# Kernel tuning notes

Measured on AMD Instinct MI355X. Metric: run time of the kernel, lower is better.

Reference implementation:

```python
import jax, jax.numpy as jnp
import numpy as np
from jax import lax

B, T, D, L, H, F = 2, 128, 256, 8, 4, 2048  # batch, time, dim, max_chunk_len, nhead, dim_feedforward
THRESH = 0.5


def setup_inputs() -> dict:
    key = jax.random.key(0)
    ks = jax.random.split(key, 12)
    s = 0.02
    nrm = lambda k, sh, sc=s: jax.random.normal(k, sh, jnp.float32) * sc
    return {
        "frames": jax.random.normal(ks[0], (B, T, D), jnp.float32),
        "cls_token": jax.random.normal(ks[1], (D,), jnp.float32),
        "Wq": nrm(ks[2], (D, D)), "bq": jnp.zeros((D,), jnp.float32),
        "Wk": nrm(ks[3], (D, D)), "bk": jnp.zeros((D,), jnp.float32),
        "Wv": nrm(ks[4], (D, D)), "bv": jnp.zeros((D,), jnp.float32),
        "Wo": nrm(ks[5], (D, D)), "bo": jnp.zeros((D,), jnp.float32),
        "ln1_g": jnp.ones((D,), jnp.float32), "ln1_b": jnp.zeros((D,), jnp.float32),
        "ln2_g": jnp.ones((D,), jnp.float32), "ln2_b": jnp.zeros((D,), jnp.float32),
        "W1": nrm(ks[6], (D, F)), "b1f": jnp.zeros((F,), jnp.float32),
        "W2": nrm(ks[7], (F, D)), "b2f": jnp.zeros((D,), jnp.float32),
        "We1": nrm(ks[8], (D, D)), "be1": jnp.zeros((D,), jnp.float32),
        "We2": jax.random.normal(ks[9], (D,), jnp.float32) * 0.1,
        "be2": jnp.zeros((), jnp.float32),
    }


def reference(frames, cls_token, Wq, bq, Wk, bk, Wv, bv, Wo, bo,
              ln1_g, ln1_b, ln2_g, ln2_b, W1, b1f, W2, b2f,
              We1, be1, We2, be2):
    """Dynamic chunker: for each start index i, grow window 1..L over frames[i:],
    run a pre-norm TransformerEncoderLayer on [CLS, window], stop at first
    p_eoc > THRESH (or window cap). Emits CLS encodings per chunk.
    Returns (chunks [B,T,D] zero-padded, counts [B])."""
    Bq, Tq, Dq = frames.shape
    dh = Dq // H
    scale = 1.0 / np.sqrt(dh).astype(np.float32)

    def ln(x, g, b):
        m = jnp.mean(x, -1, keepdims=True)
        v = jnp.var(x, -1, keepdims=True)
        return (x - m) * lax.rsqrt(v + 1e-5) * g + b

    def enc_cls(seq, kp):
        # seq: (1+L, D); kp: (1+L,) True = padded key. norm_first encoder layer.
        S = seq.shape[0]
        h = ln(seq, ln1_g, ln1_b)
        q = (h @ Wq + bq).reshape(S, H, dh)
        k = (h @ Wk + bk).reshape(S, H, dh)
        v = (h @ Wv + bv).reshape(S, H, dh)
        scores = jnp.einsum('qhd,khd->hqk', q, k) * scale
        scores = jnp.where(kp[None, None, :], -1e30, scores)
        a = jax.nn.softmax(scores, axis=-1)
        o = jnp.einsum('hqk,khd->qhd', a, v).reshape(S, Dq)
        x = seq + o @ Wo + bo
        h2 = ln(x, ln2_g, ln2_b)
        x = x + jax.nn.relu(h2 @ W1 + b1f) @ W2 + b2f
        return x[0]  # CLS position

    pos = jnp.arange(L)
    ls = jnp.arange(1, L + 1)

    def run(fpad):  # fpad: (T+L, D), one sample
        def step(i, _):
            win = lax.dynamic_slice(fpad, (i, 0), (L, Dq))           # frames[i:i+L] (zero-padded past T)
            seq = jnp.concatenate([cls_token[None, :], win], 0)     # (1+L, D)
            base_pad = (i + pos) >= Tq                               # positions past end of sequence
            kp = jnp.concatenate(
                [jnp.zeros((L, 1), bool),
                 (pos[None, :] >= ls[:, None]) | base_pad[None, :]], 1)  # (L, 1+L) one mask per candidate len
            enc = jax.vmap(enc_cls, in_axes=(None, 0))(seq, kp)      # (L, D) candidate CLS encodings
            p = jax.nn.sigmoid(jax.nn.relu(enc @ We1 + be1) @ We2 + be2)  # (L,) eoc probs
            lmax = jnp.clip(Tq - i, 1, L)
            stop = (p > THRESH) & (ls <= lmax)
            lstar = jnp.where(stop.any(), jnp.argmax(stop) + 1, lmax)
            active = i < Tq
            chunk = jnp.where(active, enc[lstar - 1], jnp.zeros((Dq,), seq.dtype))
            i_new = jnp.where(active, i + lstar.astype(i.dtype), i)
            return i_new, (chunk, active)

        _, (chunks, act) = lax.scan(step, jnp.int32(0), None, length=Tq)
        return chunks, act

    fpadded = jnp.pad(frames, ((0, 0), (0, L), (0, 0)))
    chunks, act = jax.vmap(run)(fpadded)
    counts = act.sum(-1).astype(jnp.int32)
    return chunks, counts
```

## Files before the change

kernel.cpp:

```cpp
#include <hip/hip_runtime.h>

#define DEV __device__ __forceinline__

constexpr int Bc = 2, Tc = 128, Dc = 256, Lc = 8, Hc = 4, DH = 64, Fc = 2048;
constexpr float EPS = 1e-5f, SCALE = 0.125f;
constexpr int NROWS = Bc * Tc * Lc;
constexpr int SLAB = NROWS * Dc;

constexpr int OFF_K     = 0;
constexpr int OFF_VWOH  = OFF_K + Bc * Tc * Dc;
constexpr int OFF_QCLS  = OFF_VWOH + Bc * Tc * Hc * Dc;
constexpr int OFF_KCLS  = OFF_QCLS + Dc;
constexpr int OFF_VWOHC = OFF_KCLS + Dc;
constexpr int OFF_X0    = OFF_VWOHC + Hc * Dc;
constexpr int OFF_ENC   = OFF_X0;
constexpr int OFF_H2    = OFF_X0 + SLAB;
constexpr int OFF_UP    = OFF_H2 + SLAB;
constexpr int OFF_Z     = OFF_UP + 4 * SLAB;

DEV int imin(int a, int b) { return a < b ? a : b; }

DEV float blockReduceSum(float v, float* red) {
#pragma unroll
  for (int off = 32; off; off >>= 1) v += __shfl_down(v, off, 64);
  const int lane = threadIdx.x & 63;
  const int w = threadIdx.x >> 6;
  __syncthreads();
  if (lane == 0) red[w] = v;
  __syncthreads();
  return red[0] + red[1] + red[2] + red[3];
}

__global__ __launch_bounds__(256) void k_prep(
    const float* __restrict__ frames, const float* __restrict__ cls,
    const float* __restrict__ Wq, const float* __restrict__ bq,
    const float* __restrict__ Wk, const float* __restrict__ bk,
    const float* __restrict__ Wv, const float* __restrict__ bv,
    const float* __restrict__ Wo,
    const float* __restrict__ g1, const float* __restrict__ b1,
    float* __restrict__ ws) {
  __shared__ float hsm[Dc];
  __shared__ float vsm[Dc];
  __shared__ float red[4];
  const int d = threadIdx.x;
  const int r = blockIdx.x;

  const float x = (r < Bc * Tc) ? frames[r * Dc + d] : cls[d];
  const float s = blockReduceSum(x, red);
  const float m = s * (1.0f / Dc);
  const float c = x - m;
  const float var = blockReduceSum(c * c, red) * (1.0f / Dc);
  hsm[d] = c * (1.0f / sqrtf(var + EPS)) * g1[d] + b1[d];
  __syncthreads();

  float ka = bk[d], va = bv[d];
  for (int c2 = 0; c2 < Dc; ++c2) {
    const float h = hsm[c2];
    ka = fmaf(h, Wk[c2 * Dc + d], ka);
    va = fmaf(h, Wv[c2 * Dc + d], va);
  }
  if (r < Bc * Tc) ws[OFF_K + r * Dc + d] = ka;
  else             ws[OFF_KCLS + d] = ka;
  vsm[d] = va;
  __syncthreads();

#pragma unroll
  for (int hh = 0; hh < Hc; ++hh) {
    float acc = 0.f;
    for (int c2 = 0; c2 < DH; ++c2)
      acc = fmaf(vsm[hh * DH + c2], Wo[(hh * DH + c2) * Dc + d], acc);
    if (r < Bc * Tc) ws[OFF_VWOH + r * (Hc * Dc) + hh * Dc + d] = acc;
    else             ws[OFF_VWOHC + hh * Dc + d] = acc;
  }
  if (r == Bc * Tc) {
    float qa = bq[d];
    for (int c2 = 0; c2 < Dc; ++c2) qa = fmaf(hsm[c2], Wq[c2 * Dc + d], qa);
    ws[OFF_QCLS + d] = qa;
  }
}

__global__ __launch_bounds__(256) void k_attn(
    const float* __restrict__ cls, const float* __restrict__ bo,
    const float* __restrict__ g2, const float* __restrict__ b2,
    float* __restrict__ ws) {
  const int wg = blockIdx.x;
  const int i = wg & (Tc - 1);
  const int d = threadIdx.x;
  const int lmax = imin(Tc - i, Lc);
  __shared__ float sv[Hc][Lc + 1];
  __shared__ float aP[Lc][Hc][Lc + 1];
  __shared__ __align__(16) float redA[Lc][4];
  __shared__ __align__(16) float redB[Lc][4];

  const int hh = d >> 6, lane = d & 63;
  {
    const float qv = ws[OFF_QCLS + hh * DH + lane];
    for (int j = 0; j <= Lc; ++j) {
      float p = 0.f;
      if (j == 0) p = qv * ws[OFF_KCLS + hh * DH + lane];
      else if (j - 1 < lmax) p = qv * ws[OFF_K + (wg + j - 1) * Dc + hh * DH + lane];
#pragma unroll
      for (int off = 32; off; off >>= 1) p += __shfl_down(p, off, 64);
      if (lane == 0) sv[hh][j] = p * SCALE;
    }
  }
  __syncthreads();

  if (d < Lc * Hc) {
    const int l = (d >> 2) + 1, h4 = d & 3;
    if (l <= lmax) {
      float mx = -1e30f;
      for (int j = 0; j <= l; ++j) mx = fmaxf(mx, sv[h4][j]);
      float den = 0.f;
      for (int j = 0; j <= l; ++j) den += expf(sv[h4][j] - mx);
      const float inv = 1.f / den;
      for (int j = 0; j <= l; ++j) aP[l - 1][h4][j] = expf(sv[h4][j] - mx) * inv;
    }
  }
  __syncthreads();

  float x0v[Lc];
  const float base = cls[d] + bo[d];
#pragma unroll
  for (int l = 0; l < Lc; ++l) x0v[l] = base;
  for (int j = 0; j <= lmax; ++j) {
    const float* vw = (j == 0) ? (ws + OFF_VWOHC)
                               : (ws + OFF_VWOH + (wg + j - 1) * (Hc * Dc));
    for (int h4 = 0; h4 < Hc; ++h4) {
      const float w = vw[h4 * Dc + d];
      const int lstart = (j == 0) ? 1 : j;
      for (int l = lstart; l <= lmax; ++l) x0v[l - 1] = fmaf(aP[l - 1][h4][j], w, x0v[l - 1]);
    }
  }

#pragma unroll
  for (int l = 0; l < Lc; ++l) {
    float p = x0v[l];
#pragma unroll
    for (int off = 32; off; off >>= 1) p += __shfl_down(p, off, 64);
    if (lane == 0) redA[l][hh] = p;
  }
  __syncthreads();
  float mean[Lc];
#pragma unroll
  for (int l = 0; l < Lc; ++l) {
    const float4 s4 = *(const float4*)redA[l];
    mean[l] = (s4.x + s4.y + s4.z + s4.w) * (1.f / Dc);
  }
#pragma unroll
  for (int l = 0; l < Lc; ++l) {
    const float cv = x0v[l] - mean[l];
    float p = cv * cv;
#pragma unroll
    for (int off = 32; off; off >>= 1) p += __shfl_down(p, off, 64);
    if (lane == 0) redB[l][hh] = p;
  }
  __syncthreads();

  const float g2d = g2[d], b2d = b2[d];
  for (int l = 1; l <= lmax; ++l) {
    const float4 s4 = *(const float4*)redB[l - 1];
    const float var = (s4.x + s4.y + s4.z + s4.w) * (1.f / Dc);
    const float rstd = 1.f / sqrtf(var + EPS);
    const float h2 = (x0v[l - 1] - mean[l - 1]) * rstd * g2d + b2d;
    const int rowc = wg * Lc + l - 1;
    ws[OFF_X0 + rowc * Dc + d] = x0v[l - 1];
    ws[OFF_H2 + rowc * Dc + d] = h2;
  }
  for (int l = lmax + 1; l <= Lc; ++l) {
    const int rowc = wg * Lc + l - 1;
    ws[OFF_X0 + rowc * Dc + d] = 0.f;
    ws[OFF_H2 + rowc * Dc + d] = 0.f;
  }
}

__global__ __launch_bounds__(256) void k_ffn(
    const float* __restrict__ W1, const float* __restrict__ b1f,
    const float* __restrict__ W2, float* __restrict__ ws) {
  const int mtile = blockIdx.x >> 2;
  const int q = blockIdx.x & 3;
  const int r0 = mtile * 16;
  const int tid = threadIdx.x;
  __shared__ float h2s[16][Dc];
  __shared__ float ts[16][512];

  {
    const int row = tid >> 4, c0 = (tid & 15) * 16;
    const float* src = ws + OFF_H2 + (r0 + row) * Dc + c0;
#pragma unroll
    for (int j = 0; j < 4; ++j)
      *(float4*)&h2s[row][c0 + 4 * j] = *(const float4*)&src[4 * j];
  }

  const int mg = tid >> 6;
  const int lane = tid & 63;
  const int fA = q * 512 + lane * 4;
  const int fB = fA + 256;

  float t[4][8];
  {
    const float4 bA = *(const float4*)&b1f[fA];
    const float4 bB = *(const float4*)&b1f[fB];
#pragma unroll
    for (int r = 0; r < 4; ++r) {
      t[r][0] = bA.x; t[r][1] = bA.y; t[r][2] = bA.z; t[r][3] = bA.w;
      t[r][4] = bB.x; t[r][5] = bB.y; t[r][6] = bB.z; t[r][7] = bB.w;
    }
  }
  for (int c = 0; c < Dc; c += 4) {
    float4 wA[4], wB[4];
#pragma unroll
    for (int k = 0; k < 4; ++k) {
      wA[k] = *(const float4*)&W1[(c + k) * Fc + fA];
      wB[k] = *(const float4*)&W1[(c + k) * Fc + fB];
    }
#pragma unroll
    for (int r = 0; r < 4; ++r) {
      const float4 h = *(const float4*)&h2s[mg * 4 + r][c];
      const float hv[4] = {h.x, h.y, h.z, h.w};
#pragma unroll
      for (int k = 0; k < 4; ++k) {
        t[r][0] = fmaf(hv[k], wA[k].x, t[r][0]);
        t[r][1] = fmaf(hv[k], wA[k].y, t[r][1]);
        t[r][2] = fmaf(hv[k], wA[k].z, t[r][2]);
        t[r][3] = fmaf(hv[k], wA[k].w, t[r][3]);
        t[r][4] = fmaf(hv[k], wB[k].x, t[r][4]);
        t[r][5] = fmaf(hv[k], wB[k].y, t[r][5]);
        t[r][6] = fmaf(hv[k], wB[k].z, t[r][6]);
        t[r][7] = fmaf(hv[k], wB[k].w, t[r][7]);
      }
    }
  }
#pragma unroll
  for (int r = 0; r < 4; ++r) {
    float4 vA, vB;
    vA.x = fmaxf(t[r][0], 0.f); vA.y = fmaxf(t[r][1], 0.f);
    vA.z = fmaxf(t[r][2], 0.f); vA.w = fmaxf(t[r][3], 0.f);
    vB.x = fmaxf(t[r][4], 0.f); vB.y = fmaxf(t[r][5], 0.f);
    vB.z = fmaxf(t[r][6], 0.f); vB.w = fmaxf(t[r][7], 0.f);
    *(float4*)&ts[mg * 4 + r][lane * 4] = vA;
    *(float4*)&ts[mg * 4 + r][256 + lane * 4] = vB;
  }

  const int d4 = lane * 4;
  float u[4][4];
#pragma unroll
  for (int r = 0; r < 4; ++r) { u[r][0] = 0.f; u[r][1] = 0.f; u[r][2] = 0.f; u[r][3] = 0.f; }
  for (int k = 0; k < 512; k += 4) {
    float4 wv[4];
#pragma unroll
    for (int kk = 0; kk < 4; ++kk)
      wv[kk] = *(const float4*)&W2[(q * 512 + k + kk) * Dc + d4];
#pragma unroll
    for (int r = 0; r < 4; ++r) {
      const float4 h = *(const float4*)&ts[mg * 4 + r][k];
      const float hv[4] = {h.x, h.y, h.z, h.w};
#pragma unroll
      for (int kk = 0; kk < 4; ++kk) {
        u[r][0] = fmaf(hv[kk], wv[kk].x, u[r][0]);
        u[r][1] = fmaf(hv[kk], wv[kk].y, u[r][1]);
        u[r][2] = fmaf(hv[kk], wv[kk].z, u[r][2]);
        u[r][3] = fmaf(hv[kk], wv[kk].w, u[r][3]);
      }
    }
  }
  float* up = ws + OFF_UP + q * SLAB;
#pragma unroll
  for (int r = 0; r < 4; ++r) {
    float4 v; v.x = u[r][0]; v.y = u[r][1]; v.z = u[r][2]; v.w = u[r][3];
    *(float4*)&up[(r0 + mg * 4 + r) * Dc + d4] = v;
  }
}

__global__ __launch_bounds__(256) void k_encz(
    const float* __restrict__ We1, const float* __restrict__ be1,
    const float* __restrict__ We2, const float* __restrict__ be2,
    const float* __restrict__ b2f, float* __restrict__ ws) {
  const int r0 = blockIdx.x * 8;
  const int f = threadIdx.x;
  __shared__ float encs[8][Dc];
  __shared__ __align__(16) float red[8][4];
  const float bb = b2f[f];
#pragma unroll
  for (int r = 0; r < 8; ++r) {
    const int row = r0 + r;
    const float e = ws[OFF_X0 + row * Dc + f] +
                    ws[OFF_UP + 0 * SLAB + row * Dc + f] +
                    ws[OFF_UP + 1 * SLAB + row * Dc + f] +
                    ws[OFF_UP + 2 * SLAB + row * Dc + f] +
                    ws[OFF_UP + 3 * SLAB + row * Dc + f] + bb;
    ws[OFF_ENC + row * Dc + f] = e;
    encs[r][f] = e;
  }
  __syncthreads();

  float g[8];
  const float be1f = be1[f];
#pragma unroll
  for (int r = 0; r < 8; ++r) g[r] = be1f;
  for (int c = 0; c < Dc; ++c) {
    const float w = We1[c * Dc + f];
#pragma unroll
    for (int r = 0; r < 8; ++r) g[r] = fmaf(encs[r][c], w, g[r]);
  }
  const float w2 = We2[f];
  const int lane = f & 63, wv = f >> 6;
#pragma unroll
  for (int r = 0; r < 8; ++r) {
    float p = fmaxf(g[r], 0.f) * w2;
#pragma unroll
    for (int off = 32; off; off >>= 1) p += __shfl_down(p, off, 64);
    if (lane == 0) red[r][wv] = p;
  }
  __syncthreads();
  if (f < 8) {
    const float4 s4 = *(const float4*)red[f];
    ws[OFF_Z + r0 + f] = s4.x + s4.y + s4.z + s4.w + be2[0];
  }
}

__global__ __launch_bounds__(256) void k_emit(float* __restrict__ ws, float* __restrict__ out) {
  const int b = blockIdx.x;
  const int tid = threadIdx.x;
  __shared__ int lst[Tc];
  __shared__ int path[Tc];
  __shared__ int cnt_s;
  if (tid < Tc) {
    const int i = tid;
    const int lmax = imin(Tc - i, Lc);
    const float* z = ws + OFF_Z + (b * Tc + i) * Lc;
    int ls = lmax;
    for (int l = 1; l <= lmax; ++l) {
      if (z[l - 1] > 0.f) { ls = l; break; }
    }
    lst[tid] = ls;
  }
  __syncthreads();
  if (tid < 64) {
    const int a0 = lst[tid], a1 = lst[64 + tid];
    int cur = 0, s = 0;
    while (cur < Tc) {
      const int l = (cur < 64) ? __shfl(a0, cur, 64) : __shfl(a1, cur - 64, 64);
      if (tid == 0) path[s] = cur * Lc + l - 1;
      ++s;
      cur += l;
    }
    if (tid == 0) cnt_s = s;
  }
  __syncthreads();
  const int c = cnt_s;
  for (int s0 = 0; s0 < Tc; s0 += 8) {
    float v[8];
#pragma unroll
    for (int k = 0; k < 8; ++k) {
      const int s = s0 + k;
      v[k] = (s < c) ? ws[OFF_ENC + (b * Tc * Lc + path[s]) * Dc + tid] : 0.f;
    }
#pragma unroll
    for (int k = 0; k < 8; ++k) out[(b * Tc + s0 + k) * Dc + tid] = v[k];
  }
  if (tid == 0) out[Bc * Tc * Dc + b] = (float)c;
}

extern "C" void kernel_launch(void* const* d_in, const int* in_sizes, int n_in,
                              void* d_out, int out_size, void* d_ws, size_t ws_size,
                              hipStream_t stream) {
  const float* frames = (const float*)d_in[0];
  const float* cls    = (const float*)d_in[1];
  const float* Wq     = (const float*)d_in[2];
  const float* bq     = (const float*)d_in[3];
  const float* Wk     = (const float*)d_in[4];
  const float* bk     = (const float*)d_in[5];
  const float* Wv     = (const float*)d_in[6];
  const float* bv     = (const float*)d_in[7];
  const float* Wo     = (const float*)d_in[8];
  const float* bo     = (const float*)d_in[9];
  const float* g1     = (const float*)d_in[10];
  const float* b1     = (const float*)d_in[11];
  const float* g2     = (const float*)d_in[12];
  const float* b2     = (const float*)d_in[13];
  const float* W1     = (const float*)d_in[14];
  const float* b1f    = (const float*)d_in[15];
  const float* W2     = (const float*)d_in[16];
  const float* b2f    = (const float*)d_in[17];
  const float* We1    = (const float*)d_in[18];
  const float* be1    = (const float*)d_in[19];
  const float* We2    = (const float*)d_in[20];
  const float* be2    = (const float*)d_in[21];
  float* ws = (float*)d_ws;
  float* out = (float*)d_out;

  k_prep<<<Bc * Tc + 1, 256, 0, stream>>>(frames, cls, Wq, bq, Wk, bk, Wv, bv, Wo, g1, b1, ws);
  k_attn<<<Bc * Tc, 256, 0, stream>>>(cls, bo, g2, b2, ws);
  k_ffn<<<512, 256, 0, stream>>>(W1, b1f, W2, ws);
  k_encz<<<NROWS / 8, 256, 0, stream>>>(We1, be1, We2, be2, b2f, ws);
  k_emit<<<Bc, 256, 0, stream>>>(ws, out);
}
```

Measured before the change: 253.9 us.

## Fuse FFN and end-of-chunk head into one kernel with in-block reduction

Merges the FFN kernel and the encoder/EOC-score kernel into a single 512-thread kernel. Each block now handles 8 rows over the full 2048-wide hidden dimension, where before four blocks each took a 512-wide quarter of 16 rows. The partial W2 sums are reduced in shared memory, so the four 'UP' partial slabs no longer round-trip through global memory and one launch disappears. In exchange, each block streams all of W1 and W2 for only 8 rows, so weight reuse per block is halved, and per-thread register pressure goes up.

```diff
diff --git a/kernel.cpp b/kernel.cpp
--- a/kernel.cpp
+++ b/kernel.cpp
@@ -15,8 +15,7 @@
 constexpr int OFF_X0    = OFF_VWOHC + Hc * Dc;
 constexpr int OFF_ENC   = OFF_X0;
 constexpr int OFF_H2    = OFF_X0 + SLAB;
-constexpr int OFF_UP    = OFF_H2 + SLAB;
-constexpr int OFF_Z     = OFF_UP + 4 * SLAB;
+constexpr int OFF_Z     = OFF_H2 + SLAB;
 
 DEV int imin(int a, int b) { return a < b ? a : b; }
 
@@ -174,148 +173,150 @@
   }
 }
 
-__global__ __launch_bounds__(256) void k_ffn(
+__global__ __launch_bounds__(512) void k_ffn(
     const float* __restrict__ W1, const float* __restrict__ b1f,
-    const float* __restrict__ W2, float* __restrict__ ws) {
-  const int mtile = blockIdx.x >> 2;
-  const int q = blockIdx.x & 3;
-  const int r0 = mtile * 16;
-  const int tid = threadIdx.x;
-  __shared__ float h2s[16][Dc];
-  __shared__ float ts[16][512];
-
-  {
-    const int row = tid >> 4, c0 = (tid & 15) * 16;
-    const float* src = ws + OFF_H2 + (r0 + row) * Dc + c0;
-#pragma unroll
-    for (int j = 0; j < 4; ++j)
-      *(float4*)&h2s[row][c0 + 4 * j] = *(const float4*)&src[4 * j];
-  }
-
-  const int mg = tid >> 6;
-  const int lane = tid & 63;
-  const int fA = q * 512 + lane * 4;
-  const int fB = fA + 256;
-
-  float t[4][8];
-  {
-    const float4 bA = *(const float4*)&b1f[fA];
-    const float4 bB = *(const float4*)&b1f[fB];
-#pragma unroll
-    for (int r = 0; r < 4; ++r) {
-      t[r][0] = bA.x; t[r][1] = bA.y; t[r][2] = bA.z; t[r][3] = bA.w;
-      t[r][4] = bB.x; t[r][5] = bB.y; t[r][6] = bB.z; t[r][7] = bB.w;
-    }
-  }
-  for (int c = 0; c < Dc; c += 4) {
-    float4 wA[4], wB[4];
-#pragma unroll
-    for (int k = 0; k < 4; ++k) {
-      wA[k] = *(const float4*)&W1[(c + k) * Fc + fA];
-      wB[k] = *(const float4*)&W1[(c + k) * Fc + fB];
-    }
-#pragma unroll
-    for (int r = 0; r < 4; ++r) {
-      const float4 h = *(const float4*)&h2s[mg * 4 + r][c];
-      const float hv[4] = {h.x, h.y, h.z, h.w};
-#pragma unroll
-      for (int k = 0; k < 4; ++k) {
-        t[r][0] = fmaf(hv[k], wA[k].x, t[r][0]);
-        t[r][1] = fmaf(hv[k], wA[k].y, t[r][1]);
-        t[r][2] = fmaf(hv[k], wA[k].z, t[r][2]);
-        t[r][3] = fmaf(hv[k], wA[k].w, t[r][3]);
-        t[r][4] = fmaf(hv[k], wB[k].x, t[r][4]);
-        t[r][5] = fmaf(hv[k], wB[k].y, t[r][5]);
-        t[r][6] = fmaf(hv[k], wB[k].z, t[r][6]);
-        t[r][7] = fmaf(hv[k], wB[k].w, t[r][7]);
-      }
-    }
-  }
-#pragma unroll
-  for (int r = 0; r < 4; ++r) {
-    float4 vA, vB;
-    vA.x = fmaxf(t[r][0], 0.f); vA.y = fmaxf(t[r][1], 0.f);
-    vA.z = fmaxf(t[r][2], 0.f); vA.w = fmaxf(t[r][3], 0.f);
-    vB.x = fmaxf(t[r][4], 0.f); vB.y = fmaxf(t[r][5], 0.f);
-    vB.z = fmaxf(t[r][6], 0.f); vB.w = fmaxf(t[r][7], 0.f);
-    *(float4*)&ts[mg * 4 + r][lane * 4] = vA;
-    *(float4*)&ts[mg * 4 + r][256 + lane * 4] = vB;
-  }
-
-  const int d4 = lane * 4;
-  float u[4][4];
-#pragma unroll
-  for (int r = 0; r < 4; ++r) { u[r][0] = 0.f; u[r][1] = 0.f; u[r][2] = 0.f; u[r][3] = 0.f; }
-  for (int k = 0; k < 512; k += 4) {
-    float4 wv[4];
-#pragma unroll
-    for (int kk = 0; kk < 4; ++kk)
-      wv[kk] = *(const float4*)&W2[(q * 512 + k + kk) * Dc + d4];
-#pragma unroll
-    for (int r = 0; r < 4; ++r) {
-      const float4 h = *(const float4*)&ts[mg * 4 + r][k];
-      const float hv[4] = {h.x, h.y, h.z, h.w};
-#pragma unroll
-      for (int kk = 0; kk < 4; ++kk) {
-        u[r][0] = fmaf(hv[kk], wv[kk].x, u[r][0]);
-        u[r][1] = fmaf(hv[kk], wv[kk].y, u[r][1]);
-        u[r][2] = fmaf(hv[kk], wv[kk].z, u[r][2]);
-        u[r][3] = fmaf(hv[kk], wv[kk].w, u[r][3]);
-      }
-    }
-  }
-  float* up = ws + OFF_UP + q * SLAB;
-#pragma unroll
-  for (int r = 0; r < 4; ++r) {
-    float4 v; v.x = u[r][0]; v.y = u[r][1]; v.z = u[r][2]; v.w = u[r][3];
-    *(float4*)&up[(r0 + mg * 4 + r) * Dc + d4] = v;
-  }
-}
-
-__global__ __launch_bounds__(256) void k_encz(
+    const float* __restrict__ W2, const float* __restrict__ b2f,
     const float* __restrict__ We1, const float* __restrict__ be1,
     const float* __restrict__ We2, const float* __restrict__ be2,
-    const float* __restrict__ b2f, float* __restrict__ ws) {
+    float* __restrict__ ws) {
   const int r0 = blockIdx.x * 8;
-  const int f = threadIdx.x;
-  __shared__ float encs[8][Dc];
-  __shared__ __align__(16) float red[8][4];
-  const float bb = b2f[f];
-#pragma unroll
-  for (int r = 0; r < 8; ++r) {
-    const int row = r0 + r;
-    const float e = ws[OFF_X0 + row * Dc + f] +
-                    ws[OFF_UP + 0 * SLAB + row * Dc + f] +
-                    ws[OFF_UP + 1 * SLAB + row * Dc + f] +
-                    ws[OFF_UP + 2 * SLAB + row * Dc + f] +
-                    ws[OFF_UP + 3 * SLAB + row * Dc + f] + bb;
-    ws[OFF_ENC + row * Dc + f] = e;
-    encs[r][f] = e;
-  }
-  __syncthreads();
-
-  float g[8];
-  const float be1f = be1[f];
-#pragma unroll
-  for (int r = 0; r < 8; ++r) g[r] = be1f;
-  for (int c = 0; c < Dc; ++c) {
-    const float w = We1[c * Dc + f];
-#pragma unroll
-    for (int r = 0; r < 8; ++r) g[r] = fmaf(encs[r][c], w, g[r]);
-  }
-  const float w2 = We2[f];
-  const int lane = f & 63, wv = f >> 6;
-#pragma unroll
-  for (int r = 0; r < 8; ++r) {
-    float p = fmaxf(g[r], 0.f) * w2;
-#pragma unroll
-    for (int off = 32; off; off >>= 1) p += __shfl_down(p, off, 64);
-    if (lane == 0) red[r][wv] = p;
-  }
-  __syncthreads();
-  if (f < 8) {
-    const float4 s4 = *(const float4*)red[f];
-    ws[OFF_Z + r0 + f] = s4.x + s4.y + s4.z + s4.w + be2[0];
+  const int tid = threadIdx.x;
+  const int wv = tid >> 6, lane = tid & 63;
+  __shared__ float ts[8][1024];
+  __shared__ float h2s[8][256];
+  __shared__ float encs[8][256];
+  __shared__ float zred[8][4];
+
+  *(float4*)&h2s[wv][lane * 4] =
+      *(const float4*)&ws[OFF_H2 + (r0 + wv) * Dc + lane * 4];
+  __syncthreads();
+
+  float u[8][4];
+#pragma unroll
+  for (int r = 0; r < 8; ++r) { u[r][0] = 0.f; u[r][1] = 0.f; u[r][2] = 0.f; u[r][3] = 0.f; }
+
+  for (int half = 0; half < 2; ++half) {
+    const int fg = half * 1024 + tid * 2;
+    float t[8][2];
+    {
+      const float2 bb = *(const float2*)&b1f[fg];
+#pragma unroll
+      for (int r = 0; r < 8; ++r) { t[r][0] = bb.x; t[r][1] = bb.y; }
+    }
+    for (int c = 0; c < Dc; c += 4) {
+      float2 wv1[4];
+#pragma unroll
+      for (int k = 0; k < 4; ++k) wv1[k] = *(const float2*)&W1[(c + k) * Fc + fg];
+#pragma unroll
+      for (int r = 0; r < 8; ++r) {
+        const float4 h = *(const float4*)&h2s[r][c];
+        const float hv[4] = {h.x, h.y, h.z, h.w};
+#pragma unroll
+        for (int k = 0; k < 4; ++k) {
+          t[r][0] = fmaf(hv[k], wv1[k].x, t[r][0]);
+          t[r][1] = fmaf(hv[k], wv1[k].y, t[r][1]);
+        }
+      }
+    }
+    __syncthreads();
+#pragma unroll
+    for (int r = 0; r < 8; ++r) {
+      float2 v; v.x = fmaxf(t[r][0], 0.f); v.y = fmaxf(t[r][1], 0.f);
+      *(float2*)&ts[r][tid * 2] = v;
+    }
+    __syncthreads();
+
+    for (int kk = 0; kk < 128; kk += 4) {
+      const int kl = wv * 128 + kk;
+      const int kg = half * 1024 + kl;
+      float4 wv2[4];
+#pragma unroll
+      for (int k = 0; k < 4; ++k)
+        wv2[k] = *(const float4*)&W2[(kg + k) * Dc + lane * 4];
+#pragma unroll
+      for (int r = 0; r < 8; ++r) {
+        const float4 h = *(const float4*)&ts[r][kl];
+        const float hv[4] = {h.x, h.y, h.z, h.w};
+#pragma unroll
+        for (int k = 0; k < 4; ++k) {
+          u[r][0] = fmaf(hv[k], wv2[k].x, u[r][0]);
+          u[r][1] = fmaf(hv[k], wv2[k].y, u[r][1]);
+          u[r][2] = fmaf(hv[k], wv2[k].z, u[r][2]);
+          u[r][3] = fmaf(hv[k], wv2[k].w, u[r][3]);
+        }
+      }
+    }
+    __syncthreads();
+  }
+
+  float* redb = &ts[0][0];
+  if (wv < 4) {
+#pragma unroll
+    for (int r = 0; r < 8; ++r) {
+      float4 v; v.x = u[r][0]; v.y = u[r][1]; v.z = u[r][2]; v.w = u[r][3];
+      *(float4*)&redb[(wv * 8 + r) * 256 + lane * 4] = v;
+    }
+  }
+  __syncthreads();
+  if (wv >= 4) {
+#pragma unroll
+    for (int r = 0; r < 8; ++r) {
+      float4 p = *(float4*)&redb[((wv - 4) * 8 + r) * 256 + lane * 4];
+      p.x += u[r][0]; p.y += u[r][1]; p.z += u[r][2]; p.w += u[r][3];
+      *(float4*)&redb[((wv - 4) * 8 + r) * 256 + lane * 4] = p;
+    }
+  }
+  __syncthreads();
+
+  {
+    const int r = wv, d4 = lane * 4;
+    float4 s = *(const float4*)&redb[(0 * 8 + r) * 256 + d4];
+    const float4 s1 = *(const float4*)&redb[(1 * 8 + r) * 256 + d4];
+    const float4 s2 = *(const float4*)&redb[(2 * 8 + r) * 256 + d4];
+    const float4 s3 = *(const float4*)&redb[(3 * 8 + r) * 256 + d4];
+    s.x = ((s.x + s1.x) + s2.x) + s3.x;
+    s.y = ((s.y + s1.y) + s2.y) + s3.y;
+    s.z = ((s.z + s1.z) + s2.z) + s3.z;
+    s.w = ((s.w + s1.w) + s2.w) + s3.w;
+    const float4 x0 = *(const float4*)&ws[OFF_X0 + (r0 + r) * Dc + d4];
+    const float4 bb = *(const float4*)&b2f[d4];
+    float4 e;
+    e.x = (x0.x + s.x) + bb.x; e.y = (x0.y + s.y) + bb.y;
+    e.z = (x0.z + s.z) + bb.z; e.w = (x0.w + s.w) + bb.w;
+    *(float4*)&ws[OFF_ENC + (r0 + r) * Dc + d4] = e;
+    *(float4*)&encs[r][d4] = e;
+  }
+  __syncthreads();
+
+  {
+    const int f = tid & 255;
+    const int rh = tid >> 8;
+    float g[4];
+    const float be1f = be1[f];
+#pragma unroll
+    for (int rr = 0; rr < 4; ++rr) g[rr] = be1f;
+    for (int c = 0; c < Dc; ++c) {
+      const float w = We1[c * Dc + f];
+#pragma unroll
+      for (int rr = 0; rr < 4; ++rr) g[rr] = fmaf(encs[rh * 4 + rr][c], w, g[rr]);
+    }
+    const float w2 = We2[f];
+#pragma unroll
+    for (int rr = 0; rr < 4; ++rr) {
+      float p = fmaxf(g[rr], 0.f) * w2;
+#pragma unroll
+      for (int off = 32; off; off >>= 1) p += __shfl_down(p, off, 64);
+      if (lane == 0) zred[wv][rr] = p;
+    }
+  }
+  __syncthreads();
+  if (tid < 8) {
+    const int r = tid;
+    const int wb = (r < 4) ? 0 : 4;
+    const int rl = r & 3;
+    const float z = ((zred[wb + 0][rl] + zred[wb + 1][rl]) + zred[wb + 2][rl]) +
+                    zred[wb + 3][rl];
+    ws[OFF_Z + blockIdx.x * 8 + r] = z + be2[0];
   }
 }
 
@@ -392,7 +393,6 @@
 
   k_prep<<<Bc * Tc + 1, 256, 0, stream>>>(frames, cls, Wq, bq, Wk, bk, Wv, bv, Wo, g1, b1, ws);
   k_attn<<<Bc * Tc, 256, 0, stream>>>(cls, bo, g2, b2, ws);
-  k_ffn<<<512, 256, 0, stream>>>(W1, b1f, W2, ws);
-  k_encz<<<NROWS / 8, 256, 0, stream>>>(We1, be1, We2, be2, b2f, ws);
+  k_ffn<<<NROWS / 8, 512, 0, stream>>>(W1, b1f, W2, b2f, We1, be1, We2, be2, ws);
   k_emit<<<Bc, 256, 0, stream>>>(ws, out);
 }
```

Result: no change. 253.1 us (-0.3%).
